# Performance work log

Measured on AMD Instinct MI355X. Metric: run time of the kernel, lower is better.

Reference implementation:

```python
import jax, jax.numpy as jnp
import numpy as np

H, N2, R = 512, 16, 32   # hidden_dim, state_dim//2, dt_rank=ceil(512/16)
B, L = 1, 4096


def setup_inputs() -> dict:
    key = jax.random.key(0)
    ks = jax.random.split(key, 7)
    u = jax.random.normal(ks[0], (B, L, H), dtype=jnp.float32)
    # Parameter initialization mirroring S4DKernel.__init__
    A_log = jnp.zeros((H, N2), jnp.float32)                      # log(ones)
    A_im = jnp.broadcast_to(jnp.arange(N2, dtype=jnp.float32), (H, N2)).copy()
    B_param = jax.random.normal(ks[1], (H, N2, 2), jnp.float32)
    C_param = jax.random.normal(ks[2], (H, N2, 2), jnp.float32)
    D = jax.random.normal(ks[3], (H,), jnp.float32)
    dt_w = jax.random.normal(ks[4], (H, R), jnp.float32) / np.sqrt(R)
    dt_min, dt_max, dt_floor = 1e-3, 0.1, 1e-4
    dt_init = jnp.exp(jax.random.uniform(ks[5], (H,), jnp.float32)
                      * (np.log(dt_max) - np.log(dt_floor)) + np.log(dt_floor))
    dt_init = jnp.maximum(dt_init, dt_min)
    dt_b = dt_init + jnp.log(-jnp.expm1(-dt_init))               # inverse-softplus init
    xproj_w = jax.random.normal(ks[6], (R, H), jnp.float32) / np.sqrt(H)
    return {"u": u, "A_log": A_log, "A_im": A_im, "B_param": B_param,
            "C_param": C_param, "D": D, "dt_w": dt_w, "dt_b": dt_b,
            "xproj_w": xproj_w}


def reference(u, A_log, A_im, B_param, C_param, D, dt_w, dt_b, xproj_w):
    # Complex continuous-time parameters
    A = -jnp.exp(A_log) + 1j * A_im                 # [H, N2]
    Bc = B_param[..., 0] + 1j * B_param[..., 1]     # [H, N2]
    Cc = C_param[..., 0] + 1j * C_param[..., 1]     # [H, N2]

    # dt path: x_proj_for_dt (no bias) -> dt_proj -> softplus
    dt_u = jnp.einsum('blh,rh->blr', u, xproj_w)                    # [B,L,R]
    dt = jax.nn.softplus(jnp.einsum('blr,hr->blh', dt_u, dt_w) + dt_b)  # [B,L,H]

    # ZOH discretization
    z = dt[..., None] * A                           # [B,L,H,N2] complex
    A_bar = jnp.exp(z)
    B_bar_div = jnp.where(jnp.abs(z) < 1e-4, 1.0 + z / 2, (jnp.exp(z) - 1.0) / z)
    ub = u[..., None].astype(A_bar.dtype) * B_bar_div * Bc          # [B,L,H,N2]

    # Parallel scan for h_k = A_k * h_{k-1} + u_k (first-order linear recurrence)
    def op(c1, c2):
        a1, b1 = c1
        a2, b2 = c2
        return a1 * a2, a2 * b1 + b2
    _, h = jax.lax.associative_scan(op, (A_bar, ub), axis=1)        # [B,L,H,N2]

    y = jnp.einsum('blhn,hn->blh', h, Cc) + u * D
    return y.real
```

## Files before the change

kernel.cpp:

```cpp
#include <hip/hip_runtime.h>

#define Hd 512
#define N2d 16
#define Rd 32
#define Ld 4096
#define NCHUNK 256
#define CLEN (Ld / NCHUNK)
#define NCH (Hd * N2d)
#define NGRP 16
#define NGROUPS (NCHUNK / NGRP)

__device__ __forceinline__ bool load_consts4(const float* A_log, const float* A_im,
        const float* B_param, int hnb,
        float* Are, float* Aim, float* BAr, float* BAi) {
    #pragma unroll
    for (int j = 0; j < 4; ++j) {
        int hn = hnb + j;
        Are[j] = -__expf(A_log[hn]);
        Aim[j] = A_im[hn];
        float Bre = B_param[2 * hn];
        float Bim = B_param[2 * hn + 1];
        float inv = __builtin_amdgcn_rcpf(Are[j] * Are[j] + Aim[j] * Aim[j]);
        BAr[j] = (Bre * Are[j] + Bim * Aim[j]) * inv;
        BAi[j] = (Bim * Are[j] - Bre * Aim[j]) * inv;
    }
    float d1 = Aim[1] - Aim[0], d2 = Aim[2] - Aim[1], d3 = Aim[3] - Aim[2];
    return (Are[1] == Are[0]) && (Are[2] == Are[0]) && (Are[3] == Are[0]) &&
           (d1 == d2) && (d2 == d3);
}

__global__ __launch_bounds__(256) void k_dt(const float* __restrict__ u,
                                            const float* __restrict__ xproj_w,
                                            const float* __restrict__ dt_w,
                                            const float* __restrict__ dt_b,
                                            float2* __restrict__ du_out) {
    __shared__ float u_s[8][Hd];
    __shared__ float dtu_s[8][Rd];
    const int t = threadIdx.x;
    const int l0 = blockIdx.x * 8;

    #pragma unroll
    for (int i = 0; i < 16; ++i) {
        int idx = t + i * 256;
        ((float*)u_s)[idx] = u[l0 * Hd + idx];
    }
    __syncthreads();

    const int r = t >> 3;
    const int j = t & 7;
    float part[8];
    #pragma unroll
    for (int l = 0; l < 8; ++l) part[l] = 0.f;
    for (int k = 0; k < 64; ++k) {
        float w = xproj_w[r * Hd + k * 8 + j];
        #pragma unroll
        for (int l = 0; l < 8; ++l) part[l] = fmaf(u_s[l][k * 8 + j], w, part[l]);
    }
    #pragma unroll
    for (int off = 1; off < 8; off <<= 1) {
        #pragma unroll
        for (int l = 0; l < 8; ++l) part[l] += __shfl_xor(part[l], off);
    }
    if (j == 0) {
        #pragma unroll
        for (int l = 0; l < 8; ++l) dtu_s[l][r] = part[l];
    }
    __syncthreads();

    #pragma unroll
    for (int hb = 0; hb < 2; ++hb) {
        int h = hb * 256 + t;
        float bias = dt_b[h];
        float acc[8];
        #pragma unroll
        for (int l = 0; l < 8; ++l) acc[l] = bias;
        #pragma unroll
        for (int rb = 0; rb < 8; ++rb) {
            float4 w = *(const float4*)&dt_w[h * Rd + rb * 4];
            #pragma unroll
            for (int l = 0; l < 8; ++l) {
                acc[l] = fmaf(dtu_s[l][rb * 4 + 0], w.x, acc[l]);
                acc[l] = fmaf(dtu_s[l][rb * 4 + 1], w.y, acc[l]);
                acc[l] = fmaf(dtu_s[l][rb * 4 + 2], w.z, acc[l]);
                acc[l] = fmaf(dtu_s[l][rb * 4 + 3], w.w, acc[l]);
            }
        }
        #pragma unroll
        for (int l = 0; l < 8; ++l) {
            float x = acc[l];
            float sp = fmaxf(x, 0.f) + log1pf(__expf(-fabsf(x)));
            float uv = u_s[l][h];
            float us = uv * __builtin_amdgcn_rcpf(fmaxf(sp, 1e-30f));
            du_out[(l0 + l) * Hd + h] = make_float2(sp, us);
        }
    }
}

__global__ __launch_bounds__(256) void k_chunk(const float2* __restrict__ du,
        const float* __restrict__ A_log, const float* __restrict__ A_im,
        const float* __restrict__ B_param, const float* __restrict__ C_param,
        const float* __restrict__ Dp,
        float2* __restrict__ Sb, float* __restrict__ Tc,
        float2* __restrict__ y1T) {
    const int t = threadIdx.x;
    const int q = t & 3;
    const int hh = blockIdx.y * 64 + (t >> 2);
    const int c = blockIdx.x;
    const int hnb = hh * N2d + q * 4;
    const int lbase = c * CLEN;

    float Are[4], Aim[4], BAr[4], BAi[4], Cre[4], Cim[4];
    const bool fast = load_consts4(A_log, A_im, B_param, hnb, Are, Aim, BAr, BAi);
    #pragma unroll
    for (int jj = 0; jj < 4; ++jj) {
        Cre[jj] = C_param[2 * (hnb + jj)];
        Cim[jj] = C_param[2 * (hnb + jj) + 1];
    }
    const float Dv = Dp[hh];

    float sr[4] = {0.f, 0.f, 0.f, 0.f}, si[4] = {0.f, 0.f, 0.f, 0.f};
    float sdt = 0.f;

    float2 b0[4], b1[4];

    #define LOADB(buf, bb)                                                     \
        { _Pragma("unroll")                                                    \
          for (int k = 0; k < 4; ++k)                                          \
              buf[k] = du[(lbase + (bb) * 4 + k) * Hd + hh]; }

    if (fast) {
        const float Are0 = Are[0], Aim0 = Aim[0], dA = Aim[1] - Aim[0];
        #define STEPF(buf, bb)                                                 \
            { _Pragma("unroll")                                                \
              for (int k = 0; k < 4; ++k) {                                    \
                int l = lbase + (bb) * 4 + k;                                  \
                float dtv = buf[k].x, us = buf[k].y;                           \
                sdt += dtv;                                                    \
                float er = __expf(dtv * Are0);                                 \
                float s0, c0, sd, cd;                                          \
                __sincosf(dtv * Aim0, &s0, &c0);                               \
                __sincosf(dtv * dA, &sd, &cd);                                 \
                float ar = er * c0, ai = er * s0;                              \
                float yv = 0.f;                                                \
                _Pragma("unroll")                                              \
                for (int jj = 0; jj < 4; ++jj) {                               \
                    float gr = fmaf(ar, us, -us);                              \
                    float gi = ai * us;                                        \
                    float nr = fmaf(ar, sr[jj], fmaf(-ai, si[jj],              \
                                 fmaf(gr, BAr[jj], -gi * BAi[jj])));           \
                    float ni = fmaf(ar, si[jj], fmaf( ai, sr[jj],              \
                                 fmaf(gr, BAi[jj],  gi * BAr[jj])));           \
                    sr[jj] = nr; si[jj] = ni;                                  \
                    yv = fmaf(nr, Cre[jj], fmaf(-ni, Cim[jj], yv));            \
                    if (jj < 3) {                                              \
                        float tr = fmaf(ar, cd, -ai * sd);                     \
                        ai = fmaf(ai, cd, ar * sd);                            \
                        ar = tr;                                               \
                    }                                                          \
                }                                                              \
                yv += __shfl_xor(yv, 1);                                       \
                yv += __shfl_xor(yv, 2);                                       \
                if (q == 0)                                                    \
                    y1T[l * Hd + hh] = make_float2(fmaf(dtv * us, Dv, yv), sdt);\
              } }
        LOADB(b0, 0);
        LOADB(b1, 1); STEPF(b0, 0);
        LOADB(b0, 2); STEPF(b1, 1);
        LOADB(b1, 3); STEPF(b0, 2);
        STEPF(b1, 3);
        #undef STEPF
    } else {
        #define STEPS(buf, bb)                                                 \
            { _Pragma("unroll")                                                \
              for (int k = 0; k < 4; ++k) {                                    \
                int l = lbase + (bb) * 4 + k;                                  \
                float dtv = buf[k].x, us = buf[k].y;                           \
                sdt += dtv;                                                    \
                float yv = 0.f;                                                \
                _Pragma("unroll")                                              \
                for (int jj = 0; jj < 4; ++jj) {                               \
                    float er = __expf(dtv * Are[jj]);                          \
                    float s, cc;                                               \
                    __sincosf(dtv * Aim[jj], &s, &cc);                         \
                    float ar = er * cc, ai = er * s;                           \
                    float gr = fmaf(ar, us, -us);                              \
                    float gi = ai * us;                                        \
                    float nr = fmaf(ar, sr[jj], fmaf(-ai, si[jj],              \
                                 fmaf(gr, BAr[jj], -gi * BAi[jj])));           \
                    float ni = fmaf(ar, si[jj], fmaf( ai, sr[jj],              \
                                 fmaf(gr, BAi[jj],  gi * BAr[jj])));           \
                    sr[jj] = nr; si[jj] = ni;                                  \
                    yv = fmaf(nr, Cre[jj], fmaf(-ni, Cim[jj], yv));            \
                }                                                              \
                yv += __shfl_xor(yv, 1);                                       \
                yv += __shfl_xor(yv, 2);                                       \
                if (q == 0)                                                    \
                    y1T[l * Hd + hh] = make_float2(fmaf(dtv * us, Dv, yv), sdt);\
              } }
        LOADB(b0, 0);
        LOADB(b1, 1); STEPS(b0, 0);
        LOADB(b0, 2); STEPS(b1, 1);
        LOADB(b1, 3); STEPS(b0, 2);
        STEPS(b1, 3);
        #undef STEPS
    }
    #undef LOADB

    int base = c * NCH + hnb;
    #pragma unroll
    for (int jj = 0; jj < 4; ++jj)
        Sb[base + jj] = make_float2(sr[jj], si[jj]);
    if (q == 0) Tc[c * Hd + hh] = sdt;
}

__global__ __launch_bounds__(256) void k_comb(const float2* __restrict__ Sb,
        const float* __restrict__ Tc, const float* __restrict__ A_log,
        const float* __restrict__ A_im, const float* __restrict__ C_param,
        float2* __restrict__ W, float* __restrict__ Aretab) {
    __shared__ float4 agg_s[16][NGROUPS + 1];
    __shared__ float Tc_s[NCHUNK];
    const int t = threadIdx.x;
    const int g = t >> 4;
    const int cl = t & 15;
    const int h = blockIdx.x;
    const int chain = h * N2d + cl;

    Tc_s[t] = Tc[t * Hd + h];
    __syncthreads();

    const float Are = -__expf(A_log[chain]);
    const float Aim = A_im[chain];
    if (g == 0) Aretab[chain] = Are;

    float pr[NGRP], pi[NGRP];
    float2 s[NGRP];
    #pragma unroll
    for (int i = 0; i < NGRP; ++i) {
        int c = g * NGRP + i;
        s[i] = Sb[c * NCH + chain];
        float T = Tc_s[c];
        float er = __expf(Are * T);
        float sn, cs;
        __sincosf(Aim * T, &sn, &cs);
        pr[i] = er * cs;
        pi[i] = er * sn;
    }

    float Pr = 1.f, Pi = 0.f, Hr = 0.f, Hi = 0.f;
    #pragma unroll
    for (int i = 0; i < NGRP; ++i) {
        float nhr = fmaf(pr[i], Hr, fmaf(-pi[i], Hi, s[i].x));
        float nhi = fmaf(pr[i], Hi, fmaf( pi[i], Hr, s[i].y));
        float npr = fmaf(pr[i], Pr, -pi[i] * Pi);
        float npi = fmaf(pr[i], Pi,  pi[i] * Pr);
        Hr = nhr; Hi = nhi; Pr = npr; Pi = npi;
    }
    agg_s[cl][g] = make_float4(Pr, Pi, Hr, Hi);
    __syncthreads();

    float hr = 0.f, hi = 0.f;
    for (int j = 0; j < g; ++j) {
        float4 a = agg_s[cl][j];
        float nr = fmaf(a.x, hr, fmaf(-a.y, hi, a.z));
        float ni = fmaf(a.x, hi, fmaf( a.y, hr, a.w));
        hr = nr; hi = ni;
    }

    const float Cr = C_param[2 * chain];
    const float Ci = C_param[2 * chain + 1];
    #pragma unroll
    for (int i = 0; i < NGRP; ++i) {
        int c = g * NGRP + i;
        W[c * NCH + chain] = make_float2(fmaf(Cr, hr, -Ci * hi),
                                         fmaf(Cr, hi,  Ci * hr));
        float nr = fmaf(pr[i], hr, fmaf(-pi[i], hi, s[i].x));
        float ni = fmaf(pr[i], hi, fmaf( pi[i], hr, s[i].y));
        hr = nr; hi = ni;
    }
}

__global__ __launch_bounds__(256) void k_corr(const float2* __restrict__ y1T,
        const float* __restrict__ Aretab, const float* __restrict__ A_im,
        const float2* __restrict__ W, float* __restrict__ out) {
    const int t = threadIdx.x;
    const int c = blockIdx.x;
    const int hl = t & 63;
    const int h = blockIdx.y * 64 + hl;
    const int lb = t >> 6;
    const int l0 = c * CLEN + lb * 4;
    const int hn0 = h * N2d;

    float2 yt[4];
    #pragma unroll
    for (int k = 0; k < 4; ++k) yt[k] = y1T[(l0 + k) * Hd + h];

    float2 w[N2d];
    #pragma unroll
    for (int n = 0; n < N2d; ++n) w[n] = W[c * NCH + hn0 + n];

    float are[N2d], aim[N2d];
    #pragma unroll
    for (int n = 0; n < N2d; ++n) {
        are[n] = Aretab[hn0 + n];
        aim[n] = A_im[hn0 + n];
    }
    float dA = aim[1] - aim[0];
    bool fast = true;
    #pragma unroll
    for (int n = 1; n < N2d; ++n)
        fast = fast && (are[n] == are[0]) && (aim[n] - aim[n - 1] == dA);

    if (fast) {
        const float Are0 = are[0], Aim0 = aim[0];
        #pragma unroll
        for (int k = 0; k < 4; ++k) {
            float T = yt[k].y;
            float er = __expf(Are0 * T);
            float s0, c0, sd, cd;
            __sincosf(Aim0 * T, &s0, &c0);
            __sincosf(dA * T, &sd, &cd);
            float ar = er * c0, ai = er * s0;
            float corr = 0.f;
            #pragma unroll
            for (int n = 0; n < N2d; ++n) {
                corr = fmaf(ar, w[n].x, fmaf(-ai, w[n].y, corr));
                if (n < N2d - 1) {
                    float tr = fmaf(ar, cd, -ai * sd);
                    ai = fmaf(ai, cd, ar * sd);
                    ar = tr;
                }
            }
            out[(l0 + k) * Hd + h] = yt[k].x + corr;
        }
    } else {
        #pragma unroll
        for (int k = 0; k < 4; ++k) {
            float T = yt[k].y;
            float corr = 0.f;
            #pragma unroll
            for (int n = 0; n < N2d; ++n) {
                float er = __expf(are[n] * T);
                float s, cc;
                __sincosf(aim[n] * T, &s, &cc);
                corr = fmaf(er * cc, w[n].x, fmaf(-er * s, w[n].y, corr));
            }
            out[(l0 + k) * Hd + h] = yt[k].x + corr;
        }
    }
}

extern "C" void kernel_launch(void* const* d_in, const int* in_sizes, int n_in,
                              void* d_out, int out_size, void* d_ws, size_t ws_size,
                              hipStream_t stream) {
    const float* u        = (const float*)d_in[0];
    const float* A_log    = (const float*)d_in[1];
    const float* A_im     = (const float*)d_in[2];
    const float* B_param  = (const float*)d_in[3];
    const float* C_param  = (const float*)d_in[4];
    const float* Dp       = (const float*)d_in[5];
    const float* dt_w     = (const float*)d_in[6];
    const float* dt_b     = (const float*)d_in[7];
    const float* xproj_w  = (const float*)d_in[8];

    float2* du     = (float2*)d_ws;
    float2* Sb     = du + (size_t)Ld * Hd;
    float2* W      = Sb + (size_t)NCHUNK * NCH;
    float2* y1T    = W + (size_t)NCHUNK * NCH;
    float*  Tc     = (float*)(y1T + (size_t)Ld * Hd);
    float*  Aretab = Tc + (size_t)NCHUNK * Hd;
    float*  out    = (float*)d_out;

    k_dt<<<Ld / 8, 256, 0, stream>>>(u, xproj_w, dt_w, dt_b, du);
    dim3 g2(NCHUNK, Hd / 64);
    k_chunk<<<g2, 256, 0, stream>>>(du, A_log, A_im, B_param, C_param, Dp,
                                    Sb, Tc, y1T);
    k_comb<<<Hd, 256, 0, stream>>>(Sb, Tc, A_log, A_im, C_param, W, Aretab);
    k_corr<<<g2, 256, 0, stream>>>(y1T, Aretab, A_im, W, out);
}
```

Before: 140.8 us.

## Halve chunk count, lengthen chunks, and restructure combine and correction kernels

Reduces NCHUNK from 256 to 128, so each chunk covers 32 timesteps and each thread in the chunk and correction kernels handles 8 steps instead of 4. The combine kernel now processes two hidden rows per block, reads a transposed, coalesced Tc layout, and no longer writes an Aretab table; the correction kernel recomputes Are from A_log and loads W as float4. This shrinks the Sb/W intermediate traffic and the combine work. In exchange the chunk and correction grids have half as many blocks, which lowers parallelism, and each thread runs a longer serial recurrence.

Result: faster. 132.1 us (-6.1%).

```diff
diff --git a/kernel.cpp b/kernel.cpp
--- a/kernel.cpp
+++ b/kernel.cpp
@@ -4,30 +4,11 @@
 #define N2d 16
 #define Rd 32
 #define Ld 4096
-#define NCHUNK 256
+#define NCHUNK 128
 #define CLEN (Ld / NCHUNK)
 #define NCH (Hd * N2d)
 #define NGRP 16
 #define NGROUPS (NCHUNK / NGRP)
-
-__device__ __forceinline__ bool load_consts4(const float* A_log, const float* A_im,
-        const float* B_param, int hnb,
-        float* Are, float* Aim, float* BAr, float* BAi) {
-    #pragma unroll
-    for (int j = 0; j < 4; ++j) {
-        int hn = hnb + j;
-        Are[j] = -__expf(A_log[hn]);
-        Aim[j] = A_im[hn];
-        float Bre = B_param[2 * hn];
-        float Bim = B_param[2 * hn + 1];
-        float inv = __builtin_amdgcn_rcpf(Are[j] * Are[j] + Aim[j] * Aim[j]);
-        BAr[j] = (Bre * Are[j] + Bim * Aim[j]) * inv;
-        BAi[j] = (Bim * Are[j] - Bre * Aim[j]) * inv;
-    }
-    float d1 = Aim[1] - Aim[0], d2 = Aim[2] - Aim[1], d3 = Aim[3] - Aim[2];
-    return (Are[1] == Are[0]) && (Are[2] == Are[0]) && (Are[3] == Are[0]) &&
-           (d1 == d2) && (d2 == d3);
-}
 
 __global__ __launch_bounds__(256) void k_dt(const float* __restrict__ u,
                                             const float* __restrict__ xproj_w,
@@ -109,31 +90,53 @@
     const int hnb = hh * N2d + q * 4;
     const int lbase = c * CLEN;
 
-    float Are[4], Aim[4], BAr[4], BAi[4], Cre[4], Cim[4];
-    const bool fast = load_consts4(A_log, A_im, B_param, hnb, Are, Aim, BAr, BAi);
-    #pragma unroll
-    for (int jj = 0; jj < 4; ++jj) {
-        Cre[jj] = C_param[2 * (hnb + jj)];
-        Cim[jj] = C_param[2 * (hnb + jj) + 1];
+    float alog[4], Aim[4];
+    #pragma unroll
+    for (int j = 0; j < 4; ++j) {
+        alog[j] = A_log[hnb + j];
+        Aim[j] = A_im[hnb + j];
+    }
+    float d1 = Aim[1] - Aim[0], d2 = Aim[2] - Aim[1], d3 = Aim[3] - Aim[2];
+    const bool fast = (alog[1] == alog[0]) && (alog[2] == alog[0]) &&
+                      (alog[3] == alog[0]) && (d1 == d2) && (d2 == d3);
+    float Are[4];
+    if (fast) {
+        Are[0] = -__expf(alog[0]);
+        Are[1] = Are[2] = Are[3] = Are[0];
+    } else {
+        #pragma unroll
+        for (int j = 0; j < 4; ++j) Are[j] = -__expf(alog[j]);
+    }
+    float BAr[4], BAi[4], Cre[4], Cim[4];
+    #pragma unroll
+    for (int j = 0; j < 4; ++j) {
+        int hn = hnb + j;
+        float Bre = B_param[2 * hn];
+        float Bim = B_param[2 * hn + 1];
+        float inv = __builtin_amdgcn_rcpf(Are[j] * Are[j] + Aim[j] * Aim[j]);
+        BAr[j] = (Bre * Are[j] + Bim * Aim[j]) * inv;
+        BAi[j] = (Bim * Are[j] - Bre * Aim[j]) * inv;
+        Cre[j] = C_param[2 * hn];
+        Cim[j] = C_param[2 * hn + 1];
     }
     const float Dv = Dp[hh];
 
     float sr[4] = {0.f, 0.f, 0.f, 0.f}, si[4] = {0.f, 0.f, 0.f, 0.f};
     float sdt = 0.f;
 
-    float2 b0[4], b1[4];
+    float2 b0[8], b1[8];
 
     #define LOADB(buf, bb)                                                     \
         { _Pragma("unroll")                                                    \
-          for (int k = 0; k < 4; ++k)                                          \
-              buf[k] = du[(lbase + (bb) * 4 + k) * Hd + hh]; }
+          for (int k = 0; k < 8; ++k)                                          \
+              buf[k] = du[(lbase + (bb) * 8 + k) * Hd + hh]; }
 
     if (fast) {
         const float Are0 = Are[0], Aim0 = Aim[0], dA = Aim[1] - Aim[0];
         #define STEPF(buf, bb)                                                 \
             { _Pragma("unroll")                                                \
-              for (int k = 0; k < 4; ++k) {                                    \
-                int l = lbase + (bb) * 4 + k;                                  \
+              for (int k = 0; k < 8; ++k) {                                    \
+                int l = lbase + (bb) * 8 + k;                                  \
                 float dtv = buf[k].x, us = buf[k].y;                           \
                 sdt += dtv;                                                    \
                 float er = __expf(dtv * Are0);                                 \
@@ -172,8 +175,8 @@
     } else {
         #define STEPS(buf, bb)                                                 \
             { _Pragma("unroll")                                                \
-              for (int k = 0; k < 4; ++k) {                                    \
-                int l = lbase + (bb) * 4 + k;                                  \
+              for (int k = 0; k < 8; ++k) {                                    \
+                int l = lbase + (bb) * 8 + k;                                  \
                 float dtv = buf[k].x, us = buf[k].y;                           \
                 sdt += dtv;                                                    \
                 float yv = 0.f;                                                \
@@ -210,35 +213,39 @@
     #pragma unroll
     for (int jj = 0; jj < 4; ++jj)
         Sb[base + jj] = make_float2(sr[jj], si[jj]);
-    if (q == 0) Tc[c * Hd + hh] = sdt;
+    if (q == 0) Tc[hh * NCHUNK + c] = sdt;
 }
 
 __global__ __launch_bounds__(256) void k_comb(const float2* __restrict__ Sb,
         const float* __restrict__ Tc, const float* __restrict__ A_log,
         const float* __restrict__ A_im, const float* __restrict__ C_param,
-        float2* __restrict__ W, float* __restrict__ Aretab) {
-    __shared__ float4 agg_s[16][NGROUPS + 1];
-    __shared__ float Tc_s[NCHUNK];
+        float2* __restrict__ W) {
+    __shared__ float4 agg_s[32][NGROUPS + 1];
+    __shared__ float Tc_s[2][NCHUNK];
     const int t = threadIdx.x;
-    const int g = t >> 4;
-    const int cl = t & 15;
-    const int h = blockIdx.x;
-    const int chain = h * N2d + cl;
-
-    Tc_s[t] = Tc[t * Hd + h];
+    const int g = t >> 5;
+    const int cl = t & 31;
+    const int chain = blockIdx.x * 32 + cl;
+    const int h0 = blockIdx.x * 2;
+
+    {
+        int cc = t & 127;
+        int hs = t >> 7;
+        Tc_s[hs][cc] = Tc[(h0 + hs) * NCHUNK + cc];
+    }
     __syncthreads();
 
+    const int hsel = cl >> 4;
     const float Are = -__expf(A_log[chain]);
     const float Aim = A_im[chain];
-    if (g == 0) Aretab[chain] = Are;
-
+
+    float2 s[NGRP];
     float pr[NGRP], pi[NGRP];
-    float2 s[NGRP];
     #pragma unroll
     for (int i = 0; i < NGRP; ++i) {
         int c = g * NGRP + i;
         s[i] = Sb[c * NCH + chain];
-        float T = Tc_s[c];
+        float T = Tc_s[hsel][c];
         float er = __expf(Are * T);
         float sn, cs;
         __sincosf(Aim * T, &sn, &cs);
@@ -280,40 +287,48 @@
 }
 
 __global__ __launch_bounds__(256) void k_corr(const float2* __restrict__ y1T,
-        const float* __restrict__ Aretab, const float* __restrict__ A_im,
+        const float* __restrict__ A_log, const float* __restrict__ A_im,
         const float2* __restrict__ W, float* __restrict__ out) {
     const int t = threadIdx.x;
     const int c = blockIdx.x;
     const int hl = t & 63;
     const int h = blockIdx.y * 64 + hl;
     const int lb = t >> 6;
-    const int l0 = c * CLEN + lb * 4;
+    const int l0 = c * CLEN + lb * 8;
     const int hn0 = h * N2d;
 
-    float2 yt[4];
-    #pragma unroll
-    for (int k = 0; k < 4; ++k) yt[k] = y1T[(l0 + k) * Hd + h];
+    float2 yt[8];
+    #pragma unroll
+    for (int k = 0; k < 8; ++k) yt[k] = y1T[(l0 + k) * Hd + h];
 
     float2 w[N2d];
-    #pragma unroll
-    for (int n = 0; n < N2d; ++n) w[n] = W[c * NCH + hn0 + n];
-
-    float are[N2d], aim[N2d];
+    {
+        const float4* w4 = reinterpret_cast<const float4*>(&W[c * NCH + hn0]);
+        #pragma unroll
+        for (int n = 0; n < 8; ++n) {
+            float4 v = w4[n];
+            w[2 * n]     = make_float2(v.x, v.y);
+            w[2 * n + 1] = make_float2(v.z, v.w);
+        }
+    }
+
+    float alog[N2d], aim[N2d];
     #pragma unroll
     for (int n = 0; n < N2d; ++n) {
-        are[n] = Aretab[hn0 + n];
+        alog[n] = A_log[hn0 + n];
         aim[n] = A_im[hn0 + n];
     }
     float dA = aim[1] - aim[0];
     bool fast = true;
     #pragma unroll
     for (int n = 1; n < N2d; ++n)
-        fast = fast && (are[n] == are[0]) && (aim[n] - aim[n - 1] == dA);
+        fast = fast && (alog[n] == alog[0]) && (aim[n] - aim[n - 1] == dA);
 
     if (fast) {
-        const float Are0 = are[0], Aim0 = aim[0];
-        #pragma unroll
-        for (int k = 0; k < 4; ++k) {
+        const float Are0 = -__expf(alog[0]);
+        const float Aim0 = aim[0];
+        #pragma unroll
+        for (int k = 0; k < 8; ++k) {
             float T = yt[k].y;
             float er = __expf(Are0 * T);
             float s0, c0, sd, cd;
@@ -333,8 +348,11 @@
             out[(l0 + k) * Hd + h] = yt[k].x + corr;
         }
     } else {
-        #pragma unroll
-        for (int k = 0; k < 4; ++k) {
+        float are[N2d];
+        #pragma unroll
+        for (int n = 0; n < N2d; ++n) are[n] = -__expf(alog[n]);
+        #pragma unroll
+        for (int k = 0; k < 8; ++k) {
             float T = yt[k].y;
             float corr = 0.f;
             #pragma unroll
@@ -362,18 +380,17 @@
     const float* dt_b     = (const float*)d_in[7];
     const float* xproj_w  = (const float*)d_in[8];
 
-    float2* du     = (float2*)d_ws;
-    float2* Sb     = du + (size_t)Ld * Hd;
-    float2* W      = Sb + (size_t)NCHUNK * NCH;
-    float2* y1T    = W + (size_t)NCHUNK * NCH;
-    float*  Tc     = (float*)(y1T + (size_t)Ld * Hd);
-    float*  Aretab = Tc + (size_t)NCHUNK * Hd;
-    float*  out    = (float*)d_out;
+    float2* du  = (float2*)d_ws;
+    float2* Sb  = du + (size_t)Ld * Hd;
+    float2* W   = Sb + (size_t)NCHUNK * NCH;
+    float2* y1T = W + (size_t)NCHUNK * NCH;
+    float*  Tc  = (float*)(y1T + (size_t)Ld * Hd);
+    float*  out = (float*)d_out;
 
     k_dt<<<Ld / 8, 256, 0, stream>>>(u, xproj_w, dt_w, dt_b, du);
     dim3 g2(NCHUNK, Hd / 64);
     k_chunk<<<g2, 256, 0, stream>>>(du, A_log, A_im, B_param, C_param, Dp,
                                     Sb, Tc, y1T);
-    k_comb<<<Hd, 256, 0, stream>>>(Sb, Tc, A_log, A_im, C_param, W, Aretab);
-    k_corr<<<g2, 256, 0, stream>>>(y1T, Aretab, A_im, W, out);
-}
+    k_comb<<<NCH / 32, 256, 0, stream>>>(Sb, Tc, A_log, A_im, C_param, W);
+    k_corr<<<g2, 256, 0, stream>>>(y1T, A_log, A_im, W, out);
+}
```
